# Performance work log

Hardware: AMD Instinct MI355X
Metric: run time of the kernel (lower is better)

The kernel has to match this reference:

```python
import jax, jax.numpy as jnp
import numpy as np

MIN_T = 0.1  # cfg.min_threshold
MAX_T = 0.9  # cfg.max_threshold
L = 2        # cfg.gcn_layers
B, S, D = 8, 1024, 512


def _gcn(x, adj, Ws, bs):
    # Prune/threshold the soft adjacency: keep weights in [MIN_T, MAX_T].
    adj = adj * ((adj >= MIN_T) & (adj <= MAX_T)).astype(adj.dtype)
    denom = jnp.sum(adj, axis=-1, keepdims=True) + 1.0  # +1 for self-loop
    for l in range(Ws.shape[0]):
        Ax = jnp.einsum('bxy,byd->bxd', adj, x)          # aggregate neighbors
        h = jnp.einsum('bxd,de->bxe', Ax + x, Ws[l]) + bs[l]  # self-loop + transform
        x = jax.nn.relu(h / denom)
    return x  # dropout layers are identity in eval mode


def setup_inputs() -> dict:
    key = jax.random.key(0)
    ks = jax.random.split(key, 8)
    seq_encoder_reprs = jax.random.normal(ks[0], (B, S, D), dtype=jnp.float32)
    adj_fw = jax.random.uniform(ks[1], (B, S, S), dtype=jnp.float32)
    s = 1.0 / np.sqrt(D)
    W1 = jax.random.normal(ks[2], (L, D, D), dtype=jnp.float32) * s
    b1 = jnp.zeros((L, D), dtype=jnp.float32)
    W2 = jax.random.normal(ks[3], (L, D, D), dtype=jnp.float32) * s
    b2 = jnp.zeros((L, D), dtype=jnp.float32)
    # Original zero-inits U; use small random values for a non-degenerate reference.
    U = jax.random.normal(ks[4], (1, D + 1, D + 1), dtype=jnp.float32) * 0.02
    return {"seq_encoder_reprs": seq_encoder_reprs, "adj_fw": adj_fw,
            "W1": W1, "b1": b1, "W2": W2, "b2": b2, "U": U}


def reference(seq_encoder_reprs, adj_fw, W1, b1, W2, b2, U):
    h1 = _gcn(seq_encoder_reprs, adj_fw, W1, b1)                 # forward-edge stream
    h2 = _gcn(seq_encoder_reprs, adj_fw.transpose(0, 2, 1), W2, b2)  # backward-edge stream
    r1 = jnp.concatenate([h1, jnp.ones_like(h1[..., :1])], axis=-1)  # [B,S,D+1]
    r2 = jnp.concatenate([h2, jnp.ones_like(h2[..., :1])], axis=-1)
    # 'bxi,oij,byj->boxy' then permute(0,2,3,1) -> [B,S,S,O]
    tmp = jnp.einsum('bxi,oij->boxj', r1, U)
    score = jnp.einsum('boxj,byj->boxy', tmp, r2)
    return score.transpose(0, 2, 3, 1)
```

## Files before the change

### kernel.cpp

```cpp
#include <hip/hip_runtime.h>

#define SS 1024
#define DD 512
#define BATCH 8
#define MIN_T 0.1f
#define MAX_T 0.9f

using half4  = __attribute__((ext_vector_type(4))) _Float16;
using half8  = __attribute__((ext_vector_type(8))) _Float16;
using floatx4 = __attribute__((ext_vector_type(4))) float;

typedef const __attribute__((address_space(1))) void gvoid;
typedef __attribute__((address_space(3))) void lvoid;

__global__ void mega_k(const float* __restrict__ x0, const float* __restrict__ adj,
                       const float* __restrict__ W1, const float* __restrict__ W2,
                       const float* __restrict__ U, const float* __restrict__ b1,
                       const float* __restrict__ b2,
                       _Float16* __restrict__ adjcat, _Float16* __restrict__ x0h,
                       _Float16* __restrict__ x0t, _Float16* __restrict__ Wcat,
                       _Float16* __restrict__ UT, float* __restrict__ Ubias,
                       float* __restrict__ bcat, float* __restrict__ part) {
    __shared__ float lt[64][68];
    __shared__ float csum[16][68];
    const int id = blockIdx.x;
    const int tx = threadIdx.x, ty = threadIdx.y;
    const int tid = ty * 64 + tx;
    const int i16 = tid & 15;
    const int g = tid >> 4;

    if (id < 2048) {
        int z = id >> 8, y = (id >> 4) & 15, x = id & 15;
        int r0 = y * 64, c0 = x * 64;
        const float* src = adj + (size_t)z * SS * SS;
        _Float16* dN = adjcat + (size_t)z * SS * SS;
        _Float16* dT = adjcat + (size_t)(8 + z) * SS * SS;
        const int c4 = i16 * 4;
        float colacc[4] = {};
#pragma unroll
        for (int p = 0; p < 4; ++p) {
            int r = p * 16 + g;
            floatx4 v = *(const floatx4*)&src[(size_t)(r0 + r) * SS + c0 + c4];
#pragma unroll
            for (int j = 0; j < 4; ++j) {
                float f = v[j];
                v[j] = (f >= MIN_T && f <= MAX_T) ? f : 0.f;
                colacc[j] += v[j];
            }
            half4 h = {(_Float16)v[0], (_Float16)v[1], (_Float16)v[2], (_Float16)v[3]};
            *(half4*)&dN[(size_t)(r0 + r) * SS + c0 + c4] = h;
            lt[c4][r] = v[0]; lt[c4 + 1][r] = v[1]; lt[c4 + 2][r] = v[2]; lt[c4 + 3][r] = v[3];
            float rs = v[0] + v[1] + v[2] + v[3];
#pragma unroll
            for (int m = 8; m > 0; m >>= 1) rs += __shfl_xor(rs, m, 16);
            if (i16 == 0) part[((size_t)z * SS + r0 + r) * 16 + x] = rs;
        }
        *(floatx4*)&csum[g][c4] = *(floatx4*)colacc;
        __syncthreads();
#pragma unroll
        for (int p = 0; p < 4; ++p) {
            int cc = p * 16 + g;
            int rr = c4;
            floatx4 v = *(const floatx4*)&lt[cc][rr];
            half4 h = {(_Float16)v[0], (_Float16)v[1], (_Float16)v[2], (_Float16)v[3]};
            *(half4*)&dT[(size_t)(c0 + cc) * SS + r0 + rr] = h;
        }
        if (ty == 0) {
            float cs = 0.f;
#pragma unroll
            for (int q = 0; q < 16; ++q) cs += csum[q][tx];
            part[(size_t)131072 + ((size_t)z * SS + c0 + tx) * 16 + y] = cs;
        }
    } else if (id < 3072) {
        int rel = id - 2048;
        int z = rel >> 7, y = (rel >> 3) & 15, x = rel & 7;
        int r0 = y * 64, c0 = x * 64;
        const float* src = x0 + (size_t)z * SS * DD;
        _Float16* dN = x0h + (size_t)z * SS * DD;
        _Float16* dT = x0t + (size_t)z * SS * DD;
        const int c4 = i16 * 4;
#pragma unroll
        for (int p = 0; p < 4; ++p) {
            int r = p * 16 + g;
            floatx4 v = *(const floatx4*)&src[(size_t)(r0 + r) * DD + c0 + c4];
            half4 h = {(_Float16)v[0], (_Float16)v[1], (_Float16)v[2], (_Float16)v[3]};
            *(half4*)&dN[(size_t)(r0 + r) * DD + c0 + c4] = h;
            lt[c4][r] = v[0]; lt[c4 + 1][r] = v[1]; lt[c4 + 2][r] = v[2]; lt[c4 + 3][r] = v[3];
        }
        __syncthreads();
#pragma unroll
        for (int p = 0; p < 4; ++p) {
            int cc = p * 16 + g;
            int rr = c4;
            floatx4 v = *(const floatx4*)&lt[cc][rr];
            half4 h = {(_Float16)v[0], (_Float16)v[1], (_Float16)v[2], (_Float16)v[3]};
            *(half4*)&dT[(size_t)(c0 + cc) * SS + r0 + rr] = h;
        }
    } else {
        int rel = id - 3072;
        int z = rel / 80, rem = rel % 80;
        int y = rem / 10, x = rem % 10;
        const float* src;
        _Float16* dT;
        int sld, srcR, srcC, dTR, dTC, ldT;
        if (z < 4) {
            int l = z >> 1, st = z & 1;
            src = (st ? W2 : W1) + (size_t)l * DD * DD;
            sld = DD; srcR = DD; srcC = DD;
            dT = Wcat + (size_t)z * DD * DD; ldT = DD; dTR = DD; dTC = DD;
        } else {
            src = U; sld = 513; srcR = 512; srcC = 513;
            dT = UT; ldT = DD; dTR = 640; dTC = DD;
        }
        int c0 = x * 64, r0 = y * 64;
#pragma unroll
        for (int it = 0; it < 16; ++it) {
            int r = r0 + ty + it * 4, c = c0 + tx;
            float v = 0.f;
            if (r < srcR && c < srcC) v = src[(size_t)r * sld + c];
            lt[tx][ty + it * 4] = v;
        }
        __syncthreads();
#pragma unroll
        for (int it = 0; it < 16; ++it) {
            int tr = c0 + ty + it * 4, tc = r0 + tx;
            if (tr < dTR && tc < dTC)
                dT[(size_t)tr * ldT + tc] = (_Float16)lt[ty + it * 4][tx];
        }
        if (z == 4 && x == 0 && y == 0) {
            for (int i = tid; i < 2048; i += 256) {
                int l = i >> 10, st = (i >> 9) & 1, n = i & 511;
                bcat[i] = (st == 0) ? b1[l * 512 + n] : b2[l * 512 + n];
            }
            for (int i = tid; i < 576; i += 256) Ubias[i] = (i < 513) ? U[512 * 513 + i] : 0.f;
        }
    }
}

__global__ void rsum2_k(const float* __restrict__ part, float* __restrict__ rden) {
    int row = blockIdx.x * 256 + threadIdx.x;
    const float* p = part + (size_t)row * 16;
    float s = 0.f;
#pragma unroll
    for (int i = 0; i < 16; ++i) s += p[i];
    rden[row] = 1.0f / (s + 1.0f);
}

constexpr int GBM = 128, GBN = 128, GBK = 64;

template <int EPI>
__global__ __launch_bounds__(512, 4) void gemm_k(
    const _Float16* __restrict__ A, const _Float16* __restrict__ B, void* __restrict__ Cv,
    void* __restrict__ Cv2,
    int M, int N, int K, int lda, int ldb, int ldc,
    long bA, long bB, long bC, int zmB,
    const void* __restrict__ e0, int e0ld, long bE0, int zmE,
    const float* __restrict__ e1) {
    __shared__ _Float16 lA[2][GBM * GBK];
    __shared__ _Float16 lB[2][GBN * GBK];

    const int gx = gridDim.x, gy = gridDim.y;
    const int nwg = gx * gy * gridDim.z;
    const int orig = (blockIdx.z * gy + blockIdx.y) * gx + blockIdx.x;
    const int w = (orig & 7) * (nwg >> 3) + (orig >> 3);
    const int bx = w % gx;
    const int wt = w / gx;
    const int by = wt % gy;
    const int z = wt / gy;

    A += (size_t)z * bA;
    B += (size_t)(z & zmB) * bB;
    const int m0 = bx * GBM, n0 = by * GBN;
    const int tid = threadIdx.x;
    const int lane = tid & 63, wv = tid >> 6;
    const int wr = wv >> 2, wc = wv & 3;

    auto stage = [&](int buf, int kt) {
#pragma unroll
        for (int it = 0; it < 2; ++it) {
            int q = it * 512 + tid;
            int r = q >> 3, cp = q & 7, cl = cp ^ (r & 7);
            const _Float16* g = A + (size_t)(m0 + r) * lda + kt + cl * 8;
            __builtin_amdgcn_global_load_lds((gvoid*)g,
                (lvoid*)(&lA[buf][(it * 512 + wv * 64) * 8]), 16, 0, 0);
        }
#pragma unroll
        for (int it = 0; it < 2; ++it) {
            int q = it * 512 + tid;
            int r = q >> 3, cp = q & 7, cl = cp ^ (r & 7);
            const _Float16* g = B + (size_t)(n0 + r) * ldb + kt + cl * 8;
            __builtin_amdgcn_global_load_lds((gvoid*)g,
                (lvoid*)(&lB[buf][(it * 512 + wv * 64) * 8]), 16, 0, 0);
        }
    };

    floatx4 acc[4][2] = {};

    stage(0, 0);
    asm volatile("s_waitcnt vmcnt(0)");
    __syncthreads();
    int cur = 0;
    for (int kt = 0; kt < K; kt += GBK) {
        int nxt = kt + GBK;
        if (nxt < K) stage(cur ^ 1, nxt);
#pragma unroll
        for (int kk = 0; kk < 2; ++kk) {
            half8 af[4], bf[2];
#pragma unroll
            for (int i = 0; i < 4; ++i) {
                int row = wr * 64 + i * 16 + (lane & 15);
                int cl = kk * 4 + (lane >> 4);
                int cp = cl ^ (row & 7);
                af[i] = *(const half8*)&lA[cur][row * 64 + cp * 8];
            }
#pragma unroll
            for (int j = 0; j < 2; ++j) {
                int row = wc * 32 + j * 16 + (lane & 15);
                int cl = kk * 4 + (lane >> 4);
                int cp = cl ^ (row & 7);
                bf[j] = *(const half8*)&lB[cur][row * 64 + cp * 8];
            }
#pragma unroll
            for (int i = 0; i < 4; ++i)
#pragma unroll
                for (int j = 0; j < 2; ++j)
                    acc[i][j] = __builtin_amdgcn_mfma_f32_16x16x32_f16(af[i], bf[j], acc[i][j], 0, 0, 0);
        }
        if (nxt < K) {
            asm volatile("s_waitcnt vmcnt(0)");
            __syncthreads();
        }
        cur ^= 1;
    }

    const int cm = (lane >> 4) * 4;
    const int cn = lane & 15;
    const long bAct = (long)SS * DD;
#pragma unroll
    for (int i = 0; i < 4; ++i) {
#pragma unroll
        for (int j = 0; j < 2; ++j) {
#pragma unroll
            for (int r = 0; r < 4; ++r) {
                int m = m0 + wr * 64 + i * 16 + cm + r;
                int n = n0 + wc * 32 + j * 16 + cn;
                float v = acc[i][j][r];
                if constexpr (EPI == 1) {
                    const _Float16* X = (const _Float16*)e0 + (size_t)(z & zmE) * bE0;
                    v += (float)X[(size_t)m * e0ld + n];
                    ((_Float16*)Cv)[(size_t)z * bC + (size_t)m * ldc + n] = (_Float16)v;
                } else if constexpr (EPI == 2 || EPI == 5) {
                    const float* bb = (const float*)e0 + (size_t)(z & zmE) * bE0;
                    v = (v + bb[n]) * e1[(size_t)z * e0ld + m];
                    v = v > 0.f ? v : 0.f;
                    ((_Float16*)Cv)[(size_t)z * bC + (size_t)m * ldc + n] = (_Float16)v;
                    if constexpr (EPI == 5) {
                        int bt = m >> 10, s = m & 1023;
                        ((_Float16*)Cv2)[(size_t)(z * 8 + bt) * bAct + (size_t)n * SS + s] =
                            (_Float16)v;
                    }
                } else if constexpr (EPI == 3) {
                    if (n < N) {
                        v += ((const float*)e0)[n];
                        ((_Float16*)Cv)[(size_t)z * bC + (size_t)m * ldc + n] = (_Float16)v;
                    }
                } else {
                    const _Float16* tb = (const _Float16*)e0 + (size_t)(z & zmE) * bE0;
                    v += (float)tb[(size_t)m * e0ld];
                    ((float*)Cv)[(size_t)z * bC + (size_t)m * ldc + n] = v;
                }
            }
        }
    }
}

extern "C" void kernel_launch(void* const* d_in, const int* in_sizes, int n_in,
                              void* d_out, int out_size, void* d_ws, size_t ws_size,
                              hipStream_t stream) {
    const float* x0  = (const float*)d_in[0];
    const float* adj = (const float*)d_in[1];
    const float* W1  = (const float*)d_in[2];
    const float* b1  = (const float*)d_in[3];
    const float* W2  = (const float*)d_in[4];
    const float* b2  = (const float*)d_in[5];
    const float* U   = (const float*)d_in[6];
    float* out = (float*)d_out;

    char* ws = (char*)d_ws;
    const size_t MB = 1u << 20;
    const long bAdj = (long)SS * SS, bAct = (long)SS * DD;
    const long DD2 = (long)DD * DD;
    _Float16* adjcat = (_Float16*)(ws);
    _Float16* x0t  = (_Float16*)(ws + 32 * MB);
    _Float16* x0h  = (_Float16*)(ws + 40 * MB);
    _Float16* u1   = (_Float16*)(ws + 48 * MB);
    _Float16* u2   = (_Float16*)(ws + 64 * MB);
    _Float16* u3   = (_Float16*)(ws + 80 * MB);
    _Float16* h12  = (_Float16*)(ws + 96 * MB);
    _Float16* t1h  = (_Float16*)(ws + 112 * MB);
    _Float16* Wcat = (_Float16*)(ws + 122 * MB);
    _Float16* UT   = (_Float16*)(ws + 124 * MB);
    float* Ubias   = (float*)(ws + 125 * MB);
    float* bcat    = (float*)(ws + 125 * MB + 4096);
    float* rden12  = (float*)(ws + 125 * MB + 16384);
    float* part    = (float*)(ws + 126 * MB);

    mega_k<<<3472, dim3(64, 4), 0, stream>>>(x0, adj, W1, W2, U, b1, b2,
                                             adjcat, x0h, x0t, Wcat, UT, Ubias, bcat, part);
    rsum2_k<<<64, 256, 0, stream>>>(part, rden12);

    dim3 gAgg(SS / GBM, DD / GBN, 16);
    dim3 gWmm(BATCH * SS / GBM, DD / GBN, 2);
    dim3 gT1(BATCH * SS / GBM, 5, 1);
    dim3 gSc(SS / GBM, SS / GBN, BATCH);

    gemm_k<1><<<gAgg, 512, 0, stream>>>(adjcat, x0t, u1, nullptr, SS, DD, SS, SS, SS, DD,
                                        bAdj, bAct, bAct, 7, x0h, DD, bAct, 7, nullptr);
    gemm_k<5><<<gWmm, 512, 0, stream>>>(u1, Wcat, u2, u3, BATCH * SS, DD, DD, DD, DD, DD,
                                        8 * bAct, DD2, 8 * bAct, 1,
                                        bcat, 8192, 512, 1, rden12);
    gemm_k<1><<<gAgg, 512, 0, stream>>>(adjcat, u3, u1, nullptr, SS, DD, SS, SS, SS, DD,
                                        bAdj, bAct, bAct, 15, u2, DD, bAct, 15, nullptr);
    gemm_k<2><<<gWmm, 512, 0, stream>>>(u1, Wcat + 2 * DD2, h12, nullptr,
                                        BATCH * SS, DD, DD, DD, DD, DD,
                                        8 * bAct, DD2, 8 * bAct, 1,
                                        bcat + 1024, 8192, 512, 1, rden12);

    gemm_k<3><<<gT1, 512, 0, stream>>>(h12, UT, t1h, nullptr, BATCH * SS, 576, DD, DD, DD, 576,
                                       0, 0, 0, 0, Ubias, 0, 0, 0, nullptr);
    gemm_k<4><<<gSc, 512, 0, stream>>>(t1h, h12 + 8 * bAct, out, nullptr, SS, SS, DD, 576, DD, SS,
                                       (long)SS * 576, bAct, (long)SS * SS, 15,
                                       t1h + 512, 576, (long)SS * 576, 15, nullptr);
}
```

Before: 151.3 us.

## Deepen GEMM pipeline to 4-stage K=32 ring and fold row-sum into aggregation GEMM

```diff
diff --git a/kernel.cpp b/kernel.cpp
--- a/kernel.cpp
+++ b/kernel.cpp
@@ -137,16 +137,7 @@
     }
 }
 
-__global__ void rsum2_k(const float* __restrict__ part, float* __restrict__ rden) {
-    int row = blockIdx.x * 256 + threadIdx.x;
-    const float* p = part + (size_t)row * 16;
-    float s = 0.f;
-#pragma unroll
-    for (int i = 0; i < 16; ++i) s += p[i];
-    rden[row] = 1.0f / (s + 1.0f);
-}
-
-constexpr int GBM = 128, GBN = 128, GBK = 64;
+constexpr int GBM = 128, GBN = 128, GBK = 32;
 
 template <int EPI>
 __global__ __launch_bounds__(512, 4) void gemm_k(
@@ -155,9 +146,9 @@
     int M, int N, int K, int lda, int ldb, int ldc,
     long bA, long bB, long bC, int zmB,
     const void* __restrict__ e0, int e0ld, long bE0, int zmE,
-    const float* __restrict__ e1) {
-    __shared__ _Float16 lA[2][GBM * GBK];
-    __shared__ _Float16 lB[2][GBN * GBK];
+    const float* __restrict__ e1, float* __restrict__ e2) {
+    __shared__ _Float16 lA[4][GBM * GBK];
+    __shared__ _Float16 lB[4][GBN * GBK];
 
     const int gx = gridDim.x, gy = gridDim.y;
     const int nwg = gx * gy * gridDim.z;
@@ -176,61 +167,45 @@
     const int wr = wv >> 2, wc = wv & 3;
 
     auto stage = [&](int buf, int kt) {
-#pragma unroll
-        for (int it = 0; it < 2; ++it) {
-            int q = it * 512 + tid;
-            int r = q >> 3, cp = q & 7, cl = cp ^ (r & 7);
-            const _Float16* g = A + (size_t)(m0 + r) * lda + kt + cl * 8;
-            __builtin_amdgcn_global_load_lds((gvoid*)g,
-                (lvoid*)(&lA[buf][(it * 512 + wv * 64) * 8]), 16, 0, 0);
-        }
-#pragma unroll
-        for (int it = 0; it < 2; ++it) {
-            int q = it * 512 + tid;
-            int r = q >> 3, cp = q & 7, cl = cp ^ (r & 7);
-            const _Float16* g = B + (size_t)(n0 + r) * ldb + kt + cl * 8;
-            __builtin_amdgcn_global_load_lds((gvoid*)g,
-                (lvoid*)(&lB[buf][(it * 512 + wv * 64) * 8]), 16, 0, 0);
-        }
+        int r = tid >> 2, cp = tid & 3;
+        int cl = cp ^ ((r >> 1) & 3);
+        const _Float16* ga = A + (size_t)(m0 + r) * lda + kt + cl * 8;
+        __builtin_amdgcn_global_load_lds((gvoid*)ga, (lvoid*)(&lA[buf][tid * 8]), 16, 0, 0);
+        const _Float16* gb = B + (size_t)(n0 + r) * ldb + kt + cl * 8;
+        __builtin_amdgcn_global_load_lds((gvoid*)gb, (lvoid*)(&lB[buf][tid * 8]), 16, 0, 0);
     };
 
     floatx4 acc[4][2] = {};
 
+    const int nsteps = K >> 5;
     stage(0, 0);
-    asm volatile("s_waitcnt vmcnt(0)");
-    __syncthreads();
-    int cur = 0;
-    for (int kt = 0; kt < K; kt += GBK) {
-        int nxt = kt + GBK;
-        if (nxt < K) stage(cur ^ 1, nxt);
-#pragma unroll
-        for (int kk = 0; kk < 2; ++kk) {
-            half8 af[4], bf[2];
-#pragma unroll
-            for (int i = 0; i < 4; ++i) {
-                int row = wr * 64 + i * 16 + (lane & 15);
-                int cl = kk * 4 + (lane >> 4);
-                int cp = cl ^ (row & 7);
-                af[i] = *(const half8*)&lA[cur][row * 64 + cp * 8];
-            }
-#pragma unroll
-            for (int j = 0; j < 2; ++j) {
-                int row = wc * 32 + j * 16 + (lane & 15);
-                int cl = kk * 4 + (lane >> 4);
-                int cp = cl ^ (row & 7);
-                bf[j] = *(const half8*)&lB[cur][row * 64 + cp * 8];
-            }
-#pragma unroll
-            for (int i = 0; i < 4; ++i)
-#pragma unroll
-                for (int j = 0; j < 2; ++j)
-                    acc[i][j] = __builtin_amdgcn_mfma_f32_16x16x32_f16(af[i], bf[j], acc[i][j], 0, 0, 0);
-        }
-        if (nxt < K) {
-            asm volatile("s_waitcnt vmcnt(0)");
-            __syncthreads();
-        }
-        cur ^= 1;
+    stage(1, GBK);
+    stage(2, 2 * GBK);
+    for (int k = 0; k < nsteps; ++k) {
+        if (k + 2 < nsteps)      asm volatile("s_waitcnt vmcnt(4)" ::: "memory");
+        else if (k + 1 < nsteps) asm volatile("s_waitcnt vmcnt(2)" ::: "memory");
+        else                     asm volatile("s_waitcnt vmcnt(0)" ::: "memory");
+        __builtin_amdgcn_s_barrier();
+        if (k + 3 < nsteps) stage((k + 3) & 3, (k + 3) * GBK);
+        const int cur = k & 3;
+        half8 af[4], bf[2];
+#pragma unroll
+        for (int i = 0; i < 4; ++i) {
+            int row = wr * 64 + i * 16 + (lane & 15);
+            int p = (lane >> 4) ^ ((row >> 1) & 3);
+            af[i] = *(const half8*)&lA[cur][row * 32 + p * 8];
+        }
+#pragma unroll
+        for (int j = 0; j < 2; ++j) {
+            int row = wc * 32 + j * 16 + (lane & 15);
+            int p = (lane >> 4) ^ ((row >> 1) & 3);
+            bf[j] = *(const half8*)&lB[cur][row * 32 + p * 8];
+        }
+#pragma unroll
+        for (int i = 0; i < 4; ++i)
+#pragma unroll
+            for (int j = 0; j < 2; ++j)
+                acc[i][j] = __builtin_amdgcn_mfma_f32_16x16x32_f16(af[i], bf[j], acc[i][j], 0, 0, 0);
     }
 
     const int cm = (lane >> 4) * 4;
@@ -245,7 +220,7 @@
                 int m = m0 + wr * 64 + i * 16 + cm + r;
                 int n = n0 + wc * 32 + j * 16 + cn;
                 float v = acc[i][j][r];
-                if constexpr (EPI == 1) {
+                if constexpr (EPI == 1 || EPI == 6) {
                     const _Float16* X = (const _Float16*)e0 + (size_t)(z & zmE) * bE0;
                     v += (float)X[(size_t)m * e0ld + n];
                     ((_Float16*)Cv)[(size_t)z * bC + (size_t)m * ldc + n] = (_Float16)v;
@@ -272,6 +247,16 @@
             }
         }
     }
+    if constexpr (EPI == 6) {
+        const float* part = (const float*)Cv2;
+        int row = w * 32 + (tid >> 4);
+        float s = part[(size_t)row * 16 + (tid & 15)];
+        s += __shfl_xor(s, 1, 16);
+        s += __shfl_xor(s, 2, 16);
+        s += __shfl_xor(s, 4, 16);
+        s += __shfl_xor(s, 8, 16);
+        if ((tid & 15) == 0) e2[row] = 1.0f / (s + 1.0f);
+    }
 }
 
 extern "C" void kernel_launch(void* const* d_in, const int* in_sizes, int n_in,
@@ -307,28 +292,27 @@
 
     mega_k<<<3472, dim3(64, 4), 0, stream>>>(x0, adj, W1, W2, U, b1, b2,
                                              adjcat, x0h, x0t, Wcat, UT, Ubias, bcat, part);
-    rsum2_k<<<64, 256, 0, stream>>>(part, rden12);
 
     dim3 gAgg(SS / GBM, DD / GBN, 16);
     dim3 gWmm(BATCH * SS / GBM, DD / GBN, 2);
     dim3 gT1(BATCH * SS / GBM, 5, 1);
     dim3 gSc(SS / GBM, SS / GBN, BATCH);
 
-    gemm_k<1><<<gAgg, 512, 0, stream>>>(adjcat, x0t, u1, nullptr, SS, DD, SS, SS, SS, DD,
-                                        bAdj, bAct, bAct, 7, x0h, DD, bAct, 7, nullptr);
+    gemm_k<6><<<gAgg, 512, 0, stream>>>(adjcat, x0t, u1, part, SS, DD, SS, SS, SS, DD,
+                                        bAdj, bAct, bAct, 7, x0h, DD, bAct, 7, nullptr, rden12);
     gemm_k<5><<<gWmm, 512, 0, stream>>>(u1, Wcat, u2, u3, BATCH * SS, DD, DD, DD, DD, DD,
                                         8 * bAct, DD2, 8 * bAct, 1,
-                                        bcat, 8192, 512, 1, rden12);
+                                        bcat, 8192, 512, 1, rden12, nullptr);
     gemm_k<1><<<gAgg, 512, 0, stream>>>(adjcat, u3, u1, nullptr, SS, DD, SS, SS, SS, DD,
-                                        bAdj, bAct, bAct, 15, u2, DD, bAct, 15, nullptr);
+                                        bAdj, bAct, bAct, 15, u2, DD, bAct, 15, nullptr, nullptr);
     gemm_k<2><<<gWmm, 512, 0, stream>>>(u1, Wcat + 2 * DD2, h12, nullptr,
                                         BATCH * SS, DD, DD, DD, DD, DD,
                                         8 * bAct, DD2, 8 * bAct, 1,
-                                        bcat + 1024, 8192, 512, 1, rden12);
+                                        bcat + 1024, 8192, 512, 1, rden12, nullptr);
 
     gemm_k<3><<<gT1, 512, 0, stream>>>(h12, UT, t1h, nullptr, BATCH * SS, 576, DD, DD, DD, 576,
-                                       0, 0, 0, 0, Ubias, 0, 0, 0, nullptr);
+                                       0, 0, 0, 0, Ubias, 0, 0, 0, nullptr, nullptr);
     gemm_k<4><<<gSc, 512, 0, stream>>>(t1h, h12 + 8 * bAct, out, nullptr, SS, SS, DD, 576, DD, SS,
                                        (long)SS * 576, bAct, (long)SS * SS, 15,
-                                       t1h + 512, 576, (long)SS * 576, 15, nullptr);
+                                       t1h + 512, 576, (long)SS * 576, 15, nullptr, nullptr);
 }
```

After: 164.2 us. 8.5% more time.
